# Optimization experiments

Hardware: AMD Instinct MI355X
Metric: run time of the kernel (lower is better)

The kernel has to match this reference:

```python
import jax, jax.numpy as jnp
import numpy as np


def setup_inputs() -> dict:
    key = jax.random.key(0)
    kA, kB = jax.random.split(key)
    B, H, W, C = 8, 48, 48, 256
    feature_A = jax.random.normal(kA, (B, H, W, C), dtype=jnp.float32)
    feature_B = jax.random.normal(kB, (B, H, W, C), dtype=jnp.float32)
    return {"feature_A": feature_A, "feature_B": feature_B}


def reference(feature_A, feature_B):
    # corr[b,i,j,k,l] = mean_c A[b,i,j,c] * B[b,k,l,c]
    # Expressed as a batched GEMM over the channel dim instead of the
    # naive [B,H,W,H,W,C] broadcast intermediate.
    C = feature_A.shape[-1]
    corr = jnp.einsum('bijc,bklc->bijkl', feature_A, feature_B) / C
    # L2 norm over source positions (i,j) per target position (k,l)
    penalty = jnp.sqrt(jnp.sum(corr * corr, axis=(1, 2), keepdims=True))  # [B,1,1,H,W]
    return corr / penalty
```

## Files before the change

### kernel.cpp

```cpp
#include <hip/hip_runtime.h>


#define HW2 2304
#define CH  256
#define NB  8
#define NELEM (NB * HW2 * CH)

typedef __attribute__((ext_vector_type(8))) short bf16x8;
typedef __attribute__((ext_vector_type(4))) float f32x4;

static __device__ inline unsigned short f2bf(float f) {
    union { float f; unsigned u; } x; x.f = f;
    unsigned r = x.u + 0x7FFFu + ((x.u >> 16) & 1u);
    return (unsigned short)(r >> 16);
}

static __device__ inline float bf2f(unsigned short u) {
    union { unsigned u; float f; } x; x.u = ((unsigned)u) << 16;
    return x.f;
}

static __device__ inline void async_copy16(const void* g, void* l) {
    __builtin_amdgcn_global_load_lds(
        (const __attribute__((address_space(1))) unsigned int*)g,
        (__attribute__((address_space(3))) unsigned int*)l, 16, 0, 0);
}

__global__ __launch_bounds__(256) void convert_bf16(const float* __restrict__ A,
                                                    const float* __restrict__ B,
                                                    unsigned short* __restrict__ Abf,
                                                    unsigned short* __restrict__ Bbf,
                                                    unsigned short* __restrict__ Atbf) {
    __shared__ unsigned short t[64][65];
    const int blk = blockIdx.x;
    const bool isA = blk < 1152;
    const int tb = isA ? blk : blk - 1152;
    const int b  = tb / 144;
    const int tt = tb % 144;
    const int ijt = tt >> 2, ct = tt & 3;
    const size_t base = ((size_t)b * HW2 + (size_t)ijt * 64) * CH + ct * 64;
    const float* src = (isA ? A : B) + base;
    unsigned short* dst = (isA ? Abf : Bbf) + base;
    const int tid = threadIdx.x;
    const int lr = tid & 15, rq = tid >> 4;
#pragma unroll
    for (int p = 0; p < 4; p++) {
        const int row = rq + p * 16;
        float4 v = *(const float4*)(src + (size_t)row * CH + lr * 4);
        ushort4 u;
        u.x = f2bf(v.x); u.y = f2bf(v.y); u.z = f2bf(v.z); u.w = f2bf(v.w);
        *(ushort4*)(dst + (size_t)row * CH + lr * 4) = u;
        if (isA) {
            t[row][lr * 4 + 0] = u.x; t[row][lr * 4 + 1] = u.y;
            t[row][lr * 4 + 2] = u.z; t[row][lr * 4 + 3] = u.w;
        }
    }
    if (isA) {
        __syncthreads();
#pragma unroll
        for (int p = 0; p < 4; p++) {
            const int c = rq + p * 16;
            ushort4 u;
            u.x = t[lr * 4 + 0][c]; u.y = t[lr * 4 + 1][c];
            u.z = t[lr * 4 + 2][c]; u.w = t[lr * 4 + 3][c];
            *(ushort4*)(Atbf + ((size_t)b * CH + (size_t)(ct * 64 + c)) * HW2
                        + (size_t)ijt * 64 + lr * 4) = u;
        }
    }
}

__global__ __launch_bounds__(256) void gram(const unsigned short* __restrict__ Atbf,
                                            unsigned short* __restrict__ Gbf) {
    __shared__ unsigned short As[2][4096];
    __shared__ unsigned short Bs[2][4096];
    const int tid = threadIdx.x;
    const int bx = blockIdx.x, by = blockIdx.y, b = blockIdx.z;
    const unsigned short* Ar = Atbf + ((size_t)b * CH + by * 64) * HW2;
    const unsigned short* Br = Atbf + ((size_t)b * CH + bx * 64) * HW2;
    const int srow = tid >> 2, skcol = (tid & 3) * 8;
    const int wave = tid >> 6, lane = tid & 63;
    const int wm = (wave >> 1) * 32, wn = (wave & 1) * 32;
    const int lr = lane & 15, quad = lane >> 4, k8 = quad * 8;

    f32x4 acc[2][2];
#pragma unroll
    for (int i = 0; i < 2; i++)
#pragma unroll
        for (int j = 0; j < 2; j++) acc[i][j] = (f32x4){0.f, 0.f, 0.f, 0.f};

#define G_STAGE(bufi, kt)                                                      \
    {                                                                          \
        _Pragma("unroll")                                                      \
        for (int c2 = 0; c2 < 2; c2++) {                                       \
            async_copy16(Ar + (size_t)srow * HW2 + (kt) + c2 * 32 + skcol,     \
                         &As[bufi][c2 * 2048 + tid * 8]);                      \
            async_copy16(Br + (size_t)srow * HW2 + (kt) + c2 * 32 + skcol,     \
                         &Bs[bufi][c2 * 2048 + tid * 8]);                      \
        }                                                                      \
    }

    G_STAGE(0, 0);
    __syncthreads();
    for (int t = 0; t < 36; t++) {
        const int buf = t & 1;
        if (t < 35) G_STAGE(buf ^ 1, (t + 1) * 64);
#pragma unroll
        for (int c2 = 0; c2 < 2; c2++) {
            bf16x8 af[2], bfr[2];
#pragma unroll
            for (int mt = 0; mt < 2; mt++)
                af[mt] = *(const bf16x8*)&As[buf][c2 * 2048 + (wm + mt * 16 + lr) * 32 + k8];
#pragma unroll
            for (int nt = 0; nt < 2; nt++)
                bfr[nt] = *(const bf16x8*)&Bs[buf][c2 * 2048 + (wn + nt * 16 + lr) * 32 + k8];
#pragma unroll
            for (int mt = 0; mt < 2; mt++)
#pragma unroll
                for (int nt = 0; nt < 2; nt++)
                    acc[mt][nt] = __builtin_amdgcn_mfma_f32_16x16x32_bf16(
                        af[mt], bfr[nt], acc[mt][nt], 0, 0, 0);
        }
        __syncthreads();
    }
#pragma unroll
    for (int mt = 0; mt < 2; mt++)
#pragma unroll
        for (int nt = 0; nt < 2; nt++) {
            const int row = by * 64 + wm + mt * 16 + quad * 4;
            const int col = bx * 64 + wn + nt * 16 + lr;
#pragma unroll
            for (int r = 0; r < 4; r++)
                Gbf[((size_t)b * CH + row + r) * CH + col] = f2bf(acc[mt][nt][r]);
        }
}

__global__ __launch_bounds__(256) void colsq(const unsigned short* __restrict__ Bbf,
                                             const unsigned short* __restrict__ Gbf,
                                             float* __restrict__ cs0,
                                             float* __restrict__ cs1) {
    __shared__ unsigned short As[2][4096];
    __shared__ unsigned short Bs[2][8192];
    __shared__ float colSqL[64];
    const int tid = threadIdx.x;
    const int bx = blockIdx.x;
    const int by = blockIdx.y;
    const int b  = blockIdx.z;
    const unsigned short* Ab = Bbf + ((size_t)b * HW2 + by * 64) * CH;
    const unsigned short* Gb = Gbf + ((size_t)b * CH + bx * 128) * CH;
    const int srow = tid >> 2, skcol = (tid & 3) * 8;
    const int wave = tid >> 6, lane = tid & 63;
    const int wm = (wave >> 1) * 32, wn = (wave & 1) * 64;
    const int lr = lane & 15, quad = lane >> 4, k8 = quad * 8;

    f32x4 acc[2][4];
#pragma unroll
    for (int i = 0; i < 2; i++)
#pragma unroll
        for (int j = 0; j < 4; j++) acc[i][j] = (f32x4){0.f, 0.f, 0.f, 0.f};

#define C_STAGE(bufi, kt)                                                      \
    {                                                                          \
        _Pragma("unroll")                                                      \
        for (int c2 = 0; c2 < 2; c2++) {                                       \
            async_copy16(Ab + (size_t)srow * CH + (kt) + c2 * 32 + skcol,      \
                         &As[bufi][c2 * 2048 + tid * 8]);                      \
            _Pragma("unroll")                                                  \
            for (int i = 0; i < 2; i++)                                        \
                async_copy16(Gb + (size_t)(srow + i * 64) * CH + (kt) + c2 * 32 + skcol, \
                             &Bs[bufi][c2 * 4096 + tid * 8 + i * 2048]);       \
        }                                                                      \
    }

    C_STAGE(0, 0);
    __syncthreads();
    for (int t = 0; t < 4; t++) {
        const int buf = t & 1;
        if (t < 3) C_STAGE(buf ^ 1, (t + 1) * 64);
#pragma unroll
        for (int c2 = 0; c2 < 2; c2++) {
            bf16x8 af[2], bfr[4];
#pragma unroll
            for (int mt = 0; mt < 2; mt++)
                af[mt] = *(const bf16x8*)&As[buf][c2 * 2048 + (wm + mt * 16 + lr) * 32 + k8];
#pragma unroll
            for (int nt = 0; nt < 4; nt++)
                bfr[nt] = *(const bf16x8*)&Bs[buf][c2 * 4096 + (wn + nt * 16 + lr) * 32 + k8];
#pragma unroll
            for (int mt = 0; mt < 2; mt++)
#pragma unroll
                for (int nt = 0; nt < 4; nt++)
                    acc[mt][nt] = __builtin_amdgcn_mfma_f32_16x16x32_bf16(
                        af[mt], bfr[nt], acc[mt][nt], 0, 0, 0);
        }
        __syncthreads();
    }

    if (tid < 64) colSqL[tid] = 0.f;
    __syncthreads();
#pragma unroll
    for (int mt = 0; mt < 2; mt++)
#pragma unroll
        for (int r = 0; r < 4; r++) {
            const int lrow = wm + mt * 16 + quad * 4 + r;
            float s = 0.f;
#pragma unroll
            for (int nt = 0; nt < 4; nt++) {
                const int col = bx * 128 + wn + nt * 16 + lr;
                s += acc[mt][nt][r] * bf2f(Ab[(size_t)lrow * CH + col]);
            }
            s += __shfl_xor(s, 1); s += __shfl_xor(s, 2);
            s += __shfl_xor(s, 4); s += __shfl_xor(s, 8);
            if (lr == 0) atomicAdd(&colSqL[lrow], s);
        }
    __syncthreads();
    if (tid < 64)
        (bx == 0 ? cs0 : cs1)[(size_t)b * HW2 + by * 64 + tid] = colSqL[tid];
}

__global__ __launch_bounds__(256, 2) void corr_out(const unsigned short* __restrict__ Abf,
                                                   const unsigned short* __restrict__ Bbf,
                                                   const float* __restrict__ cs0,
                                                   const float* __restrict__ cs1,
                                                   float* __restrict__ out) {
    __shared__ unsigned short As[2][4096];
    __shared__ unsigned short Bs[2][8192];
    const int tid = threadIdx.x;

    const int lin = blockIdx.x + 9 * (blockIdx.y + 18 * blockIdx.z);
    const int b  = lin & 7;
    const int r_ = lin >> 3;
    const int bx = r_ % 9;
    const int by = r_ / 9;

    const unsigned short* Ab = Abf + ((size_t)b * HW2 + (size_t)by * 128) * CH;
    const unsigned short* Bb = Bbf + ((size_t)b * HW2 + (size_t)bx * 256) * CH;

    const int srow = tid >> 2, skcol = (tid & 3) * 8;
    const int wave = tid >> 6, lane = tid & 63;
    const int wm = (wave >> 1) * 64, wn = (wave & 1) * 128;
    const int lr = lane & 15, quad = lane >> 4, k8 = quad * 8;

    f32x4 acc[4][8];
#pragma unroll
    for (int i = 0; i < 4; i++)
#pragma unroll
        for (int j = 0; j < 8; j++) acc[i][j] = (f32x4){0.f, 0.f, 0.f, 0.f};

#define O_STAGE(bufi, kt)                                                      \
    {                                                                          \
        _Pragma("unroll")                                                      \
        for (int i = 0; i < 2; i++)                                            \
            async_copy16(Ab + (size_t)(srow + i * 64) * CH + (kt) + skcol,     \
                         &As[bufi][tid * 8 + i * 2048]);                       \
        _Pragma("unroll")                                                      \
        for (int i = 0; i < 4; i++)                                            \
            async_copy16(Bb + (size_t)(srow + i * 64) * CH + (kt) + skcol,     \
                         &Bs[bufi][tid * 8 + i * 2048]);                       \
    }

    O_STAGE(0, 0);
    __syncthreads();
    for (int t = 0; t < 8; t++) {
        const int buf = t & 1;
        if (t < 7) O_STAGE(buf ^ 1, (t + 1) * 32);
        bf16x8 af[4], bfr[8];
#pragma unroll
        for (int mt = 0; mt < 4; mt++)
            af[mt] = *(const bf16x8*)&As[buf][(wm + mt * 16 + lr) * 32 + k8];
#pragma unroll
        for (int nt = 0; nt < 8; nt++)
            bfr[nt] = *(const bf16x8*)&Bs[buf][(wn + nt * 16 + lr) * 32 + k8];
#pragma unroll
        for (int mt = 0; mt < 4; mt++)
#pragma unroll
            for (int nt = 0; nt < 8; nt++)
                acc[mt][nt] = __builtin_amdgcn_mfma_f32_16x16x32_bf16(
                    af[mt], bfr[nt], acc[mt][nt], 0, 0, 0);
        __syncthreads();
    }

    const size_t outBase = (size_t)b * HW2 * HW2;
    const float* c0 = cs0 + (size_t)b * HW2;
    const float* c1 = cs1 + (size_t)b * HW2;
#pragma unroll
    for (int nt = 0; nt < 8; nt++) {
        const int col = bx * 256 + wn + nt * 16 + lr;
        const float rinv = rsqrtf(c0[col] + c1[col]);
#pragma unroll
        for (int mt = 0; mt < 4; mt++) {
            const int row0 = by * 128 + wm + mt * 16 + quad * 4;
            f32x4 v = acc[mt][nt];
#pragma unroll
            for (int r = 0; r < 4; r++)
                out[outBase + (size_t)(row0 + r) * HW2 + col] = v[r] * rinv;
        }
    }
}

extern "C" void kernel_launch(void* const* d_in, const int* in_sizes, int n_in,
                              void* d_out, int out_size, void* d_ws, size_t ws_size,
                              hipStream_t stream) {
    const float* A = (const float*)d_in[0];
    const float* B = (const float*)d_in[1];
    float* out = (float*)d_out;

    unsigned short* Abf  = (unsigned short*)d_ws;
    unsigned short* Bbf  = Abf + NELEM;
    unsigned short* Atbf = Bbf + NELEM;
    unsigned short* Gbf  = Atbf + NELEM;
    float* cs0 = (float*)(Gbf + (size_t)NB * CH * CH);
    float* cs1 = cs0 + (size_t)NB * HW2;

    convert_bf16<<<2304, 256, 0, stream>>>(A, B, Abf, Bbf, Atbf);
    gram<<<dim3(4, 4, NB), 256, 0, stream>>>(Atbf, Gbf);
    colsq<<<dim3(2, 36, NB), 256, 0, stream>>>(Bbf, Gbf, cs0, cs1);
    corr_out<<<dim3(9, 18, NB), 256, 0, stream>>>(Abf, Bbf, cs0, cs1, out);
}
```

Measured before the change: 254.6 us.

## Shrink corr_out tile to 128x128 and drop double-buffered K pipeline

The output GEMM tile is halved from 128x256 to 128x128, doubling the grid to 18x18x8 blocks with fewer accumulators per wave (16 instead of 32 MFMA tiles). The double-buffered async prefetch is replaced by a simple loop that loads 64-wide K chunks, syncs, then computes. The aim is higher occupancy and lower register pressure with more blocks, at the cost of more redundant A/B loads and no load/compute overlap inside a block. The min-blocks hint on launch_bounds is also removed.

```diff
diff --git a/kernel.cpp b/kernel.cpp
--- a/kernel.cpp
+++ b/kernel.cpp
@@ -217,74 +217,81 @@
         (bx == 0 ? cs0 : cs1)[(size_t)b * HW2 + by * 64 + tid] = colSqL[tid];
 }
 
-__global__ __launch_bounds__(256, 2) void corr_out(const unsigned short* __restrict__ Abf,
-                                                   const unsigned short* __restrict__ Bbf,
-                                                   const float* __restrict__ cs0,
-                                                   const float* __restrict__ cs1,
-                                                   float* __restrict__ out) {
-    __shared__ unsigned short As[2][4096];
-    __shared__ unsigned short Bs[2][8192];
+__global__ __launch_bounds__(256) void corr_out(const unsigned short* __restrict__ Abf,
+                                                const unsigned short* __restrict__ Bbf,
+                                                const float* __restrict__ cs0,
+                                                const float* __restrict__ cs1,
+                                                float* __restrict__ out) {
+    __shared__ unsigned short As[2 * 128 * 32];
+    __shared__ unsigned short Bs[2 * 128 * 32];
+
     const int tid = threadIdx.x;
 
-    const int lin = blockIdx.x + 9 * (blockIdx.y + 18 * blockIdx.z);
+    const int lin = blockIdx.x + 18 * (blockIdx.y + 18 * blockIdx.z);
     const int b  = lin & 7;
     const int r_ = lin >> 3;
-    const int bx = r_ % 9;
-    const int by = r_ / 9;
+    const int bx = r_ % 18;
+    const int by = r_ / 18;
 
     const unsigned short* Ab = Abf + ((size_t)b * HW2 + (size_t)by * 128) * CH;
-    const unsigned short* Bb = Bbf + ((size_t)b * HW2 + (size_t)bx * 256) * CH;
-
-    const int srow = tid >> 2, skcol = (tid & 3) * 8;
-    const int wave = tid >> 6, lane = tid & 63;
-    const int wm = (wave >> 1) * 64, wn = (wave & 1) * 128;
-    const int lr = lane & 15, quad = lane >> 4, k8 = quad * 8;
-
-    f32x4 acc[4][8];
+    const unsigned short* Bb = Bbf + ((size_t)b * HW2 + (size_t)bx * 128) * CH;
+
+    const int srow  = tid >> 2;
+    const int skcol = (tid & 3) * 8;
+
+    const int wave = tid >> 6;
+    const int lane = tid & 63;
+    const int wm   = (wave >> 1) * 64;
+    const int wn   = (wave & 1) * 64;
+    const int lr   = lane & 15;
+    const int quad = lane >> 4;
+    const int k8   = quad * 8;
+
+    f32x4 acc[4][4];
 #pragma unroll
     for (int i = 0; i < 4; i++)
 #pragma unroll
-        for (int j = 0; j < 8; j++) acc[i][j] = (f32x4){0.f, 0.f, 0.f, 0.f};
-
-#define O_STAGE(bufi, kt)                                                      \
-    {                                                                          \
-        _Pragma("unroll")                                                      \
-        for (int i = 0; i < 2; i++)                                            \
-            async_copy16(Ab + (size_t)(srow + i * 64) * CH + (kt) + skcol,     \
-                         &As[bufi][tid * 8 + i * 2048]);                       \
-        _Pragma("unroll")                                                      \
-        for (int i = 0; i < 4; i++)                                            \
-            async_copy16(Bb + (size_t)(srow + i * 64) * CH + (kt) + skcol,     \
-                         &Bs[bufi][tid * 8 + i * 2048]);                       \
-    }
-
-    O_STAGE(0, 0);
-    __syncthreads();
-    for (int t = 0; t < 8; t++) {
-        const int buf = t & 1;
-        if (t < 7) O_STAGE(buf ^ 1, (t + 1) * 32);
-        bf16x8 af[4], bfr[8];
-#pragma unroll
-        for (int mt = 0; mt < 4; mt++)
-            af[mt] = *(const bf16x8*)&As[buf][(wm + mt * 16 + lr) * 32 + k8];
-#pragma unroll
-        for (int nt = 0; nt < 8; nt++)
-            bfr[nt] = *(const bf16x8*)&Bs[buf][(wn + nt * 16 + lr) * 32 + k8];
-#pragma unroll
-        for (int mt = 0; mt < 4; mt++)
-#pragma unroll
-            for (int nt = 0; nt < 8; nt++)
-                acc[mt][nt] = __builtin_amdgcn_mfma_f32_16x16x32_bf16(
-                    af[mt], bfr[nt], acc[mt][nt], 0, 0, 0);
-        __syncthreads();
-    }
-
+        for (int j = 0; j < 4; j++) acc[i][j] = (f32x4){0.f, 0.f, 0.f, 0.f};
+
+    for (int kt = 0; kt < CH; kt += 64) {
+#pragma unroll
+        for (int c = 0; c < 2; c++) {
+            const int kof = kt + c * 32;
+#pragma unroll
+            for (int i = 0; i < 2; i++) {
+                async_copy16(Ab + (size_t)(srow + i * 64) * CH + kof + skcol,
+                             &As[c * 4096 + tid * 8 + i * 2048]);
+                async_copy16(Bb + (size_t)(srow + i * 64) * CH + kof + skcol,
+                             &Bs[c * 4096 + tid * 8 + i * 2048]);
+            }
+        }
+        __syncthreads();
+#pragma unroll
+        for (int c = 0; c < 2; c++) {
+            bf16x8 af[4], bfr[4];
+#pragma unroll
+            for (int mt = 0; mt < 4; mt++)
+                af[mt] = *(const bf16x8*)&As[c * 4096 + (wm + mt * 16 + lr) * 32 + k8];
+#pragma unroll
+            for (int nt = 0; nt < 4; nt++)
+                bfr[nt] = *(const bf16x8*)&Bs[c * 4096 + (wn + nt * 16 + lr) * 32 + k8];
+#pragma unroll
+            for (int mt = 0; mt < 4; mt++)
+#pragma unroll
+                for (int nt = 0; nt < 4; nt++)
+                    acc[mt][nt] = __builtin_amdgcn_mfma_f32_16x16x32_bf16(
+                        af[mt], bfr[nt], acc[mt][nt], 0, 0, 0);
+        }
+        __syncthreads();
+    }
+
+    const int colBase = bx * 128 + wn;
     const size_t outBase = (size_t)b * HW2 * HW2;
     const float* c0 = cs0 + (size_t)b * HW2;
     const float* c1 = cs1 + (size_t)b * HW2;
 #pragma unroll
-    for (int nt = 0; nt < 8; nt++) {
-        const int col = bx * 256 + wn + nt * 16 + lr;
+    for (int nt = 0; nt < 4; nt++) {
+        const int col = colBase + nt * 16 + lr;
         const float rinv = rsqrtf(c0[col] + c1[col]);
 #pragma unroll
         for (int mt = 0; mt < 4; mt++) {
@@ -314,5 +321,5 @@
     convert_bf16<<<2304, 256, 0, stream>>>(A, B, Abf, Bbf, Atbf);
     gram<<<dim3(4, 4, NB), 256, 0, stream>>>(Atbf, Gbf);
     colsq<<<dim3(2, 36, NB), 256, 0, stream>>>(Bbf, Gbf, cs0, cs1);
-    corr_out<<<dim3(9, 18, NB), 256, 0, stream>>>(Abf, Bbf, cs0, cs1, out);
-}
+    corr_out<<<dim3(18, 18, NB), 256, 0, stream>>>(Abf, Bbf, cs0, cs1, out);
+}
```

Result: no change. 250.1 us (-1.8%).
